# Kernel optimization log

Measured on AMD Instinct MI355X. Metric: run time of the kernel, lower is better.

## Reference

```python
import jax, jax.numpy as jnp
import numpy as np

B, C, S, E, H = 16, 24, 128, 256, 8
P = E // H  # head projection dim (consistent interpretation of the buggy source)
EPS = 1e-6


def _ln(x, g, b):
    mu = jnp.mean(x, axis=-1, keepdims=True)
    var = jnp.mean((x - mu) ** 2, axis=-1, keepdims=True)
    return (x - mu) * jax.lax.rsqrt(var + EPS) * g + b


def setup_inputs() -> dict:
    key = jax.random.key(0)
    ks = jax.random.split(key, 16)
    s = 0.02
    return {
        'x': jax.random.normal(ks[0], (B, C, S, E), jnp.float32),
        # spatial attention params
        'Wq_s': s * jax.random.normal(ks[1], (H, C, P, E), jnp.float32),
        'Wk_s': s * jax.random.normal(ks[2], (H, E, P), jnp.float32),
        'Wv_s': s * jax.random.normal(ks[3], (H, E, P), jnp.float32),
        'Wo_s': s * jax.random.normal(ks[4], (C, E, E), jnp.float32),
        # temporal attention params
        'Wq_t': s * jax.random.normal(ks[5], (H, C, E, P), jnp.float32),
        'Wk_t': s * jax.random.normal(ks[6], (H, C, E, P), jnp.float32),
        'Wv_t': s * jax.random.normal(ks[7], (H, C, E, P), jnp.float32),
        'Wo_t': s * jax.random.normal(ks[8], (C, E, E), jnp.float32),
        # shared layernorm
        'ln_g': jnp.ones((E,), jnp.float32),
        'ln_b': jnp.zeros((E,), jnp.float32),
        # per-joint pointwise FF (Linear->ReLU->Linear)
        'ff_w1': s * jax.random.normal(ks[9], (C, E, E), jnp.float32),
        'ff_b1': jnp.zeros((C, E), jnp.float32),
        'ff_w2': s * jax.random.normal(ks[10], (C, E, E), jnp.float32),
        'ff_b2': jnp.zeros((C, E), jnp.float32),
    }


def _spatial_attention(x, Wq, Wk, Wv, Wo):
    # x: [B,C,S,E]; per-head per-joint query proj, shared key/value proj
    q = jnp.einsum('bcse,hcpe->bshcp', x, Wq)          # [B,S,H,C,P]
    k = jnp.einsum('bcse,hep->bshcp', x, Wk)
    v = jnp.einsum('bcse,hep->bshcp', x, Wv)
    scores = jnp.einsum('bshcp,bshdp->bshcd', q, k) / jnp.sqrt(jnp.float32(P))
    a = jax.nn.softmax(scores, axis=-1)                # attn over joints d
    o = jnp.einsum('bshcd,bshdp->bshcp', a, v)
    o = o.transpose(0, 3, 1, 2, 4).reshape(x.shape[0], C, x.shape[2], H * P)  # [B,C,S,E]
    return jnp.einsum('bcse,cef->bcsf', o, Wo)


def _temporal_attention(x, Wq, Wk, Wv, Wo):
    q = jnp.einsum('bcse,hcep->bhcsp', x, Wq)          # [B,H,C,S,P]
    k = jnp.einsum('bcse,hcep->bhcsp', x, Wk)
    v = jnp.einsum('bcse,hcep->bhcsp', x, Wv)
    scores = jnp.einsum('bhcsp,bhctp->bhcst', q, k) / jnp.sqrt(jnp.float32(P))
    a = jax.nn.softmax(scores, axis=-1)                # attn over time t
    o = jnp.einsum('bhcst,bhctp->bhcsp', a, v)
    o = o.transpose(0, 2, 3, 1, 4).reshape(x.shape[0], C, x.shape[2], H * P)  # [B,C,S,E]
    return jnp.einsum('bcse,cef->bcsf', o, Wo)


def reference(x, Wq_s, Wk_s, Wv_s, Wo_s, Wq_t, Wk_t, Wv_t, Wo_t, ln_g, ln_b, ff_w1, ff_b1, ff_w2, ff_b2):
    spat = _spatial_attention(x, Wq_s, Wk_s, Wv_s, Wo_s)
    temp = _temporal_attention(x, Wq_t, Wk_t, Wv_t, Wo_t)
    attn_out = _ln(x + spat, ln_g, ln_b) + _ln(x + temp, ln_g, ln_b)
    # per-joint pointwise FF, vectorized over joints
    h = jax.nn.relu(jnp.einsum('bcse,cef->bcsf', attn_out, ff_w1) + ff_b1[None, :, None, :])
    ff = jnp.einsum('bcse,cef->bcsf', h, ff_w2) + ff_b2[None, :, None, :]
    return _ln(attn_out + ff, ln_g, ln_b)
```

## Files before the change

### kernel.cpp

```cpp
#include <hip/hip_runtime.h>
#include <hip/hip_bf16.h>

constexpr int Bn = 16, Cn = 24, Sn = 128, En = 256, Hn = 8, Pn = 32;
constexpr int NROWS = Bn * Cn * Sn;
constexpr size_t NBUF = (size_t)Bn * Cn * Sn * En;
constexpr size_t WSLOT = (size_t)Cn * 256 * 256;

typedef __bf16 bf16_t;
typedef bf16_t bf16x8 __attribute__((ext_vector_type(8)));
typedef bf16_t bf16x4 __attribute__((ext_vector_type(4)));
typedef float f32x4 __attribute__((ext_vector_type(4)));

__device__ __forceinline__ void gl2lds16(const bf16_t* g, bf16_t* l) {
    typedef const __attribute__((address_space(1))) unsigned int* gp_t;
    typedef __attribute__((address_space(3))) unsigned int* lp_t;
    __builtin_amdgcn_global_load_lds((gp_t)(unsigned long long)g,
                                     (lp_t)(unsigned int)(unsigned long long)l,
                                     16, 0, 0);
}

__global__ __launch_bounds__(256) void conv_x_k(const float* __restrict__ x,
                                                bf16_t* __restrict__ xb) {
    const size_t i = ((size_t)blockIdx.x * 256 + threadIdx.x) * 4;
    const float4 v = *(const float4*)(x + i);
    bf16x4 o = {(bf16_t)v.x, (bf16_t)v.y, (bf16_t)v.z, (bf16_t)v.w};
    *(bf16x4*)(xb + i) = o;
}

__global__ __launch_bounds__(256) void conv_w_copy_k(const float* __restrict__ W,
                                                     bf16_t* __restrict__ out) {
    const int row = blockIdx.x * 4 + (threadIdx.x >> 6);
    const int lane = threadIdx.x & 63;
    const int n = row & 255, c = row >> 8;
    const float* src = W + (size_t)c * (Pn * En) + (size_t)(n >> 5) * (Cn * Pn * En) +
                       (size_t)(n & 31) * En + lane * 4;
    const float4 v = *(const float4*)src;
    bf16x4 o = {(bf16_t)v.x, (bf16_t)v.y, (bf16_t)v.z, (bf16_t)v.w};
    *(bf16x4*)(out + (size_t)row * 256 + lane * 4) = o;
}

struct TDesc { const float* W; int Sc, Snh, Se; };

__global__ __launch_bounds__(256) void conv_w_tr_k(
    TDesc d0, TDesc d1, TDesc d2, TDesc d3, TDesc d4, TDesc d5, TDesc d6,
    bf16_t* __restrict__ out)
{
    TDesc d;
    switch (blockIdx.z) {
        case 0: d = d0; break; case 1: d = d1; break; case 2: d = d2; break;
        case 3: d = d3; break; case 4: d = d4; break; case 5: d = d5; break;
        default: d = d6; break;
    }
    const int g = blockIdx.x & 7, et = blockIdx.x >> 3;
    const int c = blockIdx.y;

    __shared__ float tile[32][65];

    const int t = threadIdx.x;
    const float* base = d.W + (size_t)c * d.Sc + (size_t)g * d.Snh;

#pragma unroll
    for (int pass = 0; pass < 2; ++pass) {
        const int e_local = pass * 32 + (t >> 3);
        const int j4 = (t & 7) * 4;
        const float4 v = *(const float4*)(base + (size_t)(et * 64 + e_local) * d.Se + j4);
        tile[j4 + 0][e_local] = v.x;
        tile[j4 + 1][e_local] = v.y;
        tile[j4 + 2][e_local] = v.z;
        tile[j4 + 3][e_local] = v.w;
    }
    __syncthreads();

    const int j = t >> 3, e8 = (t & 7) * 8;
    bf16x8 o;
#pragma unroll
    for (int k = 0; k < 8; ++k) o[k] = (bf16_t)tile[j][e8 + k];
    *(bf16x8*)(out + (size_t)blockIdx.z * WSLOT +
               ((size_t)c * 256 + g * 32 + j) * 256 + et * 64 + e8) = o;
}

__global__ __launch_bounds__(256) void conv_w_k(const float* __restrict__ W,
                                                bf16_t* __restrict__ Wb,
                                                int Sc, int Snh, int Snp, int Se) {
    const int n = blockIdx.x & 255, c = blockIdx.x >> 8;
    const int e = threadIdx.x;
    Wb[(size_t)blockIdx.x * 256 + e] =
        (bf16_t)W[(size_t)c * Sc + (size_t)(n >> 5) * Snh + (n & 31) * Snp + (size_t)e * Se];
}

struct GDesc { const bf16_t* W; bf16_t* O; int Aoff, Wc, Ob, Oc, Os, Onh, Onp, trans; };

template <int NP, int EPI>
__global__ __launch_bounds__(256) void gemm_mfma(
    const bf16_t* __restrict__ A, int Ab, int Ac, int As,
    GDesc g0, GDesc g1, GDesc g2, const float* __restrict__ bias)
{
    const int b = blockIdx.x, c = blockIdx.z;
    const int proj = (NP == 1) ? 0 : ((int)blockIdx.y >> 1);
    const int nt = (NP == 1) ? (int)blockIdx.y : ((int)blockIdx.y & 1);
    GDesc g = (proj == 0) ? g0 : (proj == 1) ? g1 : g2;

    __shared__ bf16_t smem[3][2][128 * 32];
    bf16_t* Cs = &smem[0][0][0];

    const int tid = threadIdx.x, wv = tid >> 6, ln = tid & 63;
    const int wm = (wv >> 1) * 64, wn = (wv & 1) * 64;
    const int lr = ln & 15, hi = ln >> 4;

    const bf16_t* Abase = A + g.Aoff + (size_t)b * Ab + (size_t)c * Ac;
    const bf16_t* Bbase = g.W + (size_t)c * g.Wc + (size_t)(nt * 128) * 256;

    auto stage = [&](int buf, int kt) {
        const int k0 = kt * 32;
#pragma unroll
        for (int it = 0; it < 2; ++it) {
            const int cb = it * 256 + wv * 64;
            const int mc = cb + ln;
            const int row = mc >> 2;
            const int kc = (((mc & 3) ^ ((row >> 1) & 3)) * 8);
            gl2lds16(Abase + (size_t)row * As + k0 + kc, &smem[buf][0][cb * 8]);
            gl2lds16(Bbase + (size_t)row * 256 + k0 + kc, &smem[buf][1][cb * 8]);
        }
    };

    f32x4 acc[4][4] = {};

    stage(0, 0);
    stage(1, 1);

#pragma unroll
    for (int kt = 0; kt < 8; ++kt) {
        if (kt < 6) stage((kt + 2) % 3, kt + 2);
        if (kt < 6)       asm volatile("s_waitcnt vmcnt(8)" ::: "memory");
        else if (kt == 6) asm volatile("s_waitcnt vmcnt(4)" ::: "memory");
        else              asm volatile("s_waitcnt vmcnt(0)" ::: "memory");
        __builtin_amdgcn_s_barrier();
        __builtin_amdgcn_sched_barrier(0);

        const int cur = kt % 3;
        bf16x8 af[4], bfr[4];
#pragma unroll
        for (int i = 0; i < 4; ++i) {
            const int r = wm + i * 16 + lr;
            af[i] = *(const bf16x8*)&smem[cur][0][r * 32 + ((hi ^ ((r >> 1) & 3)) * 8)];
        }
#pragma unroll
        for (int j = 0; j < 4; ++j) {
            const int r = wn + j * 16 + lr;
            bfr[j] = *(const bf16x8*)&smem[cur][1][r * 32 + ((hi ^ ((r >> 1) & 3)) * 8)];
        }
        __builtin_amdgcn_s_setprio(1);
#pragma unroll
        for (int i = 0; i < 4; ++i)
#pragma unroll
            for (int j = 0; j < 4; ++j)
                acc[i][j] = __builtin_amdgcn_mfma_f32_16x16x32_bf16(af[i], bfr[j], acc[i][j], 0, 0, 0);
        __builtin_amdgcn_s_setprio(0);

        __builtin_amdgcn_sched_barrier(0);
        __builtin_amdgcn_s_barrier();
    }

#pragma unroll
    for (int pass = 0; pass < 2; ++pass) {
        if (!g.trans) {
            if (wm == pass * 64) {
#pragma unroll
                for (int i = 0; i < 4; ++i)
#pragma unroll
                    for (int j = 0; j < 4; ++j) {
                        const int n = nt * 128 + wn + j * 16 + lr;
                        float bv = 0.f;
                        if (EPI) bv = bias[c * 256 + n];
#pragma unroll
                        for (int r = 0; r < 4; ++r) {
                            float v = acc[i][j][r];
                            if (EPI) { v += bv; if (EPI == 1) v = fmaxf(v, 0.f); }
                            Cs[(i * 16 + hi * 4 + r) * 136 + wn + j * 16 + lr] = (bf16_t)v;
                        }
                    }
            }
            __syncthreads();
#pragma unroll
            for (int it = 0; it < 2; ++it) {
                const int lrow = it * 32 + (tid >> 3);
                const int n0 = (tid & 7) * 16;
                bf16x8 v0 = *(const bf16x8*)&Cs[lrow * 136 + n0];
                bf16x8 v1 = *(const bf16x8*)&Cs[lrow * 136 + n0 + 8];
                const int m = pass * 64 + lrow;
                const int n = nt * 128 + n0;
                bf16_t* dst = g.O + (size_t)b * g.Ob + (size_t)c * g.Oc +
                              (size_t)m * g.Os + (size_t)(n >> 5) * g.Onh + (n & 31);
                *(bf16x8*)dst = v0;
                *(bf16x8*)(dst + 8) = v1;
            }
            __syncthreads();
        } else {
            if (wn == pass * 64) {
#pragma unroll
                for (int i = 0; i < 4; ++i)
#pragma unroll
                    for (int j = 0; j < 4; ++j) {
                        bf16x4 pk = {(bf16_t)acc[i][j][0], (bf16_t)acc[i][j][1],
                                     (bf16_t)acc[i][j][2], (bf16_t)acc[i][j][3]};
                        *(bf16x4*)&Cs[(j * 16 + lr) * 136 + wm + i * 16 + hi * 4] = pk;
                    }
            }
            __syncthreads();
#pragma unroll
            for (int it = 0; it < 2; ++it) {
                const int lrow = it * 32 + (tid >> 3);
                const int m0 = (tid & 7) * 16;
                bf16x8 v0 = *(const bf16x8*)&Cs[lrow * 136 + m0];
                bf16x8 v1 = *(const bf16x8*)&Cs[lrow * 136 + m0 + 8];
                const int n = nt * 128 + pass * 64 + lrow;
                bf16_t* dst = g.O + (size_t)b * g.Ob + (size_t)c * g.Oc +
                              (size_t)(n >> 5) * g.Onh + (size_t)(n & 31) * g.Onp + m0;
                *(bf16x8*)dst = v0;
                *(bf16x8*)(dst + 8) = v1;
            }
            __syncthreads();
        }
    }
}

__global__ __launch_bounds__(256) void attn_spatial_mfma(
    const bf16_t* __restrict__ Q, const bf16_t* __restrict__ K,
    const bf16_t* __restrict__ V, bf16_t* __restrict__ O)
{
    __shared__ bf16_t Ps[4][32 * 40];
    __shared__ bf16_t Vt[4][32 * 40];

    const int tid = threadIdx.x, wv = tid >> 6, ln = tid & 63;
    const int lr = ln & 15, hi = ln >> 4, lk = hi * 8;

    const int bsh = blockIdx.x * 4 + wv;
    const int h = bsh & 7, s = (bsh >> 3) & 127, b = bsh >> 10;
    const size_t qb = (size_t)bsh * (Cn * Pn);

    {
        const int p = ln >> 1, c0 = 24 + (ln & 1) * 4;
        bf16x4 z = {};
        *(bf16x4*)&Vt[wv][p * 40 + c0] = z;
    }
#pragma unroll
    for (int it = 0; it < 2; ++it) {
        const int ch = it * 64 + ln;
        if (ch < 96) {
            const int cc = ch >> 2, p0 = (ch & 3) * 8;
            bf16x8 v = *(const bf16x8*)(V + qb + cc * 32 + p0);
#pragma unroll
            for (int j = 0; j < 8; ++j)
                Vt[wv][(p0 + j) * 40 + cc] = v[j];
        }
    }

    bf16x8 aq0 = *(const bf16x8*)(Q + qb + lr * 32 + lk);
    bf16x8 aq1 = *(const bf16x8*)(Q + qb + (16 + lr) * 32 + lk);
    bf16x8 bk0 = *(const bf16x8*)(K + qb + lr * 32 + lk);
    bf16x8 bk1 = *(const bf16x8*)(K + qb + (16 + lr) * 32 + lk);
    const f32x4 zz = {0.f, 0.f, 0.f, 0.f};
    f32x4 sc[2][2];
    sc[0][0] = __builtin_amdgcn_mfma_f32_16x16x32_bf16(aq0, bk0, zz, 0, 0, 0);
    sc[0][1] = __builtin_amdgcn_mfma_f32_16x16x32_bf16(aq0, bk1, zz, 0, 0, 0);
    sc[1][0] = __builtin_amdgcn_mfma_f32_16x16x32_bf16(aq1, bk0, zz, 0, 0, 0);
    sc[1][1] = __builtin_amdgcn_mfma_f32_16x16x32_bf16(aq1, bk1, zz, 0, 0, 0);

    const float scale = 0.17677669529663687f;
#pragma unroll
    for (int i = 0; i < 2; ++i) {
        float s0[4], s1[4], mx[4];
#pragma unroll
        for (int r = 0; r < 4; ++r) {
            s0[r] = sc[i][0][r] * scale;
            s1[r] = (lr >= 8) ? -3.0e38f : sc[i][1][r] * scale;
            mx[r] = fmaxf(s0[r], s1[r]);
        }
#pragma unroll
        for (int d = 1; d < 16; d <<= 1)
#pragma unroll
            for (int r = 0; r < 4; ++r) mx[r] = fmaxf(mx[r], __shfl_xor(mx[r], d));
        float e0[4], e1[4], sm[4];
#pragma unroll
        for (int r = 0; r < 4; ++r) {
            e0[r] = __expf(s0[r] - mx[r]);
            e1[r] = __expf(s1[r] - mx[r]);
            sm[r] = e0[r] + e1[r];
        }
#pragma unroll
        for (int d = 1; d < 16; d <<= 1)
#pragma unroll
            for (int r = 0; r < 4; ++r) sm[r] += __shfl_xor(sm[r], d);
#pragma unroll
        for (int r = 0; r < 4; ++r) {
            const float inv = 1.f / sm[r];
            const int row = i * 16 + hi * 4 + r;
            Ps[wv][row * 40 + lr]      = (bf16_t)(e0[r] * inv);
            Ps[wv][row * 40 + 16 + lr] = (bf16_t)(e1[r] * inv);
        }
    }

    bf16x8 ap0 = *(const bf16x8*)&Ps[wv][lr * 40 + lk];
    bf16x8 ap1 = *(const bf16x8*)&Ps[wv][(16 + lr) * 40 + lk];
    bf16x8 bv0 = *(const bf16x8*)&Vt[wv][lr * 40 + lk];
    bf16x8 bv1 = *(const bf16x8*)&Vt[wv][(16 + lr) * 40 + lk];
    f32x4 o[2][2];
    o[0][0] = __builtin_amdgcn_mfma_f32_16x16x32_bf16(ap0, bv0, zz, 0, 0, 0);
    o[0][1] = __builtin_amdgcn_mfma_f32_16x16x32_bf16(ap0, bv1, zz, 0, 0, 0);
    o[1][0] = __builtin_amdgcn_mfma_f32_16x16x32_bf16(ap1, bv0, zz, 0, 0, 0);
    o[1][1] = __builtin_amdgcn_mfma_f32_16x16x32_bf16(ap1, bv1, zz, 0, 0, 0);

#pragma unroll
    for (int i = 0; i < 2; ++i)
#pragma unroll
        for (int r = 0; r < 4; ++r) {
            const int c = i * 16 + hi * 4 + r;
            if (c < 24) {
                const size_t ob = ((size_t)(b * Cn + c) * Sn + s) * En + h * Pn;
#pragma unroll
                for (int j = 0; j < 2; ++j)
                    O[ob + j * 16 + lr] = (bf16_t)o[i][j][r];
            }
        }
}

__global__ __launch_bounds__(256) void attn_temporal_mfma(
    const bf16_t* __restrict__ Q, const bf16_t* __restrict__ K,
    const bf16_t* __restrict__ Vt, bf16_t* __restrict__ O)
{
    const int c = blockIdx.x, h = blockIdx.y, b = blockIdx.z;
    const size_t base = ((size_t)(b * Hn + h) * Cn + c) * (Sn * Pn);

    __shared__ bf16_t Qs[128 * 32];
    __shared__ bf16_t Ks[128 * 32];
    __shared__ bf16_t Vs[32 * 136];
    __shared__ bf16_t Ps[128 * 136];

    const int tid = threadIdx.x, wv = tid >> 6, ln = tid & 63;
    const int lr = ln & 15, lk = (ln >> 4) * 8;

#pragma unroll
    for (int it = 0; it < 2; ++it) {
        const int cb = it * 256 + wv * 64;
        const int mc = cb + ln;
        const int row = mc >> 2, kc = (mc & 3) * 8;
        gl2lds16(Q + base + row * 32 + kc, &Qs[cb * 8]);
        gl2lds16(K + base + row * 32 + kc, &Ks[cb * 8]);
    }
#pragma unroll
    for (int it = 0; it < 2; ++it) {
        const int mc = it * 256 + tid;
        const int p = mc >> 4, scn = (mc & 15) * 8;
        bf16x8 v = *(const bf16x8*)(Vt + base + p * 128 + scn);
        *(bf16x8*)&Vs[p * 136 + scn] = v;
    }
    __syncthreads();

    const int r0 = wv * 32;
    bf16x8 aq0 = *(const bf16x8*)&Qs[(r0 + lr) * 32 + lk];
    bf16x8 aq1 = *(const bf16x8*)&Qs[(r0 + 16 + lr) * 32 + lk];
    f32x4 sc_[2][8];
    const f32x4 zz = {0.f, 0.f, 0.f, 0.f};
#pragma unroll
    for (int j = 0; j < 8; ++j) {
        bf16x8 bk = *(const bf16x8*)&Ks[(j * 16 + lr) * 32 + lk];
        sc_[0][j] = __builtin_amdgcn_mfma_f32_16x16x32_bf16(aq0, bk, zz, 0, 0, 0);
        sc_[1][j] = __builtin_amdgcn_mfma_f32_16x16x32_bf16(aq1, bk, zz, 0, 0, 0);
    }

    const float scale = 0.17677669529663687f;
#pragma unroll
    for (int i = 0; i < 2; ++i) {
        float mx[4], sm[4];
#pragma unroll
        for (int r = 0; r < 4; ++r) {
            float m = sc_[i][0][r];
#pragma unroll
            for (int j = 1; j < 8; ++j) m = fmaxf(m, sc_[i][j][r]);
            mx[r] = m;
        }
#pragma unroll
        for (int d = 1; d < 16; d <<= 1)
#pragma unroll
            for (int r = 0; r < 4; ++r) mx[r] = fmaxf(mx[r], __shfl_xor(mx[r], d));
#pragma unroll
        for (int r = 0; r < 4; ++r) sm[r] = 0.f;
#pragma unroll
        for (int j = 0; j < 8; ++j)
#pragma unroll
            for (int r = 0; r < 4; ++r) {
                const float e = __expf((sc_[i][j][r] - mx[r]) * scale);
                sc_[i][j][r] = e; sm[r] += e;
            }
#pragma unroll
        for (int d = 1; d < 16; d <<= 1)
#pragma unroll
            for (int r = 0; r < 4; ++r) sm[r] += __shfl_xor(sm[r], d);
        float inv[4];
#pragma unroll
        for (int r = 0; r < 4; ++r) inv[r] = 1.f / sm[r];
        const int rb = r0 + i * 16 + (ln >> 4) * 4;
#pragma unroll
        for (int j = 0; j < 8; ++j)
#pragma unroll
            for (int r = 0; r < 4; ++r)
                Ps[(rb + r) * 136 + j * 16 + lr] = (bf16_t)(sc_[i][j][r] * inv[r]);
    }
    __syncthreads();

    f32x4 o[2][2] = {};
#pragma unroll
    for (int kk = 0; kk < 4; ++kk) {
        bf16x8 ap0 = *(const bf16x8*)&Ps[(r0 + lr) * 136 + kk * 32 + lk];
        bf16x8 ap1 = *(const bf16x8*)&Ps[(r0 + 16 + lr) * 136 + kk * 32 + lk];
        bf16x8 bv0 = *(const bf16x8*)&Vs[lr * 136 + kk * 32 + lk];
        bf16x8 bv1 = *(const bf16x8*)&Vs[(16 + lr) * 136 + kk * 32 + lk];
        o[0][0] = __builtin_amdgcn_mfma_f32_16x16x32_bf16(ap0, bv0, o[0][0], 0, 0, 0);
        o[0][1] = __builtin_amdgcn_mfma_f32_16x16x32_bf16(ap0, bv1, o[0][1], 0, 0, 0);
        o[1][0] = __builtin_amdgcn_mfma_f32_16x16x32_bf16(ap1, bv0, o[1][0], 0, 0, 0);
        o[1][1] = __builtin_amdgcn_mfma_f32_16x16x32_bf16(ap1, bv1, o[1][1], 0, 0, 0);
    }

#pragma unroll
    for (int i = 0; i < 2; ++i) {
        const int sb = r0 + i * 16 + (ln >> 4) * 4;
#pragma unroll
        for (int j = 0; j < 2; ++j) {
            const int p = h * 32 + j * 16 + lr;
#pragma unroll
            for (int r = 0; r < 4; ++r)
                O[((size_t)(b * Cn + c) * Sn + (sb + r)) * En + p] = (bf16_t)o[i][j][r];
        }
    }
}

__global__ __launch_bounds__(256) void ln_combine_k(
    const bf16_t* __restrict__ xb, const bf16_t* __restrict__ spat,
    const bf16_t* __restrict__ temp, const float* __restrict__ g,
    const float* __restrict__ beta, bf16_t* __restrict__ AO)
{
    const int row = blockIdx.x * 4 + (threadIdx.x >> 6);
    const int lane = threadIdx.x & 63;
    const size_t off = (size_t)row * En;

    float v1[4], v2[4];
    float s1 = 0, s2 = 0, q1 = 0, q2 = 0;
#pragma unroll
    for (int i = 0; i < 4; i++) {
        const int e = lane + i * 64;
        const float xv = (float)xb[off + e];
        const float a = xv + (float)spat[off + e];
        const float t = xv + (float)temp[off + e];
        v1[i] = a; v2[i] = t;
        s1 += a; s2 += t; q1 += a * a; q2 += t * t;
    }
    for (int d = 32; d; d >>= 1) {
        s1 += __shfl_xor(s1, d); s2 += __shfl_xor(s2, d);
        q1 += __shfl_xor(q1, d); q2 += __shfl_xor(q2, d);
    }
    const float mu1 = s1 / En, mu2 = s2 / En;
    const float r1 = rsqrtf(q1 / En - mu1 * mu1 + 1e-6f);
    const float r2 = rsqrtf(q2 / En - mu2 * mu2 + 1e-6f);
#pragma unroll
    for (int i = 0; i < 4; i++) {
        const int e = lane + i * 64;
        const float out = (v1[i] - mu1) * r1 * g[e] + beta[e] +
                          (v2[i] - mu2) * r2 * g[e] + beta[e];
        AO[off + e] = (bf16_t)out;
    }
}

__global__ __launch_bounds__(256) void ln_final_k(
    const bf16_t* __restrict__ AO, const bf16_t* __restrict__ FF,
    const float* __restrict__ g, const float* __restrict__ beta,
    float* __restrict__ out)
{
    const int row = blockIdx.x * 4 + (threadIdx.x >> 6);
    const int lane = threadIdx.x & 63;
    const size_t off = (size_t)row * En;

    float v[4];
    float s = 0, q = 0;
#pragma unroll
    for (int i = 0; i < 4; i++) {
        const int e = lane + i * 64;
        const float a = (float)AO[off + e] + (float)FF[off + e];
        v[i] = a; s += a; q += a * a;
    }
    for (int d = 32; d; d >>= 1) { s += __shfl_xor(s, d); q += __shfl_xor(q, d); }
    const float mu = s / En;
    const float r = rsqrtf(q / En - mu * mu + 1e-6f);
#pragma unroll
    for (int i = 0; i < 4; i++) {
        const int e = lane + i * 64;
        out[off + e] = (v[i] - mu) * r * g[e] + beta[e];
    }
}

extern "C" void kernel_launch(void* const* d_in, const int* in_sizes, int n_in,
                              void* d_out, int out_size, void* d_ws, size_t ws_size,
                              hipStream_t stream)
{
    const float* x     = (const float*)d_in[0];
    const float* Wq_s  = (const float*)d_in[1];
    const float* Wk_s  = (const float*)d_in[2];
    const float* Wv_s  = (const float*)d_in[3];
    const float* Wo_s  = (const float*)d_in[4];
    const float* Wq_t  = (const float*)d_in[5];
    const float* Wk_t  = (const float*)d_in[6];
    const float* Wv_t  = (const float*)d_in[7];
    const float* Wo_t  = (const float*)d_in[8];
    const float* ln_g  = (const float*)d_in[9];
    const float* ln_b  = (const float*)d_in[10];
    const float* ff_w1 = (const float*)d_in[11];
    const float* ff_b1 = (const float*)d_in[12];
    const float* ff_w2 = (const float*)d_in[13];
    const float* ff_b2 = (const float*)d_in[14];
    float* out = (float*)d_out;

    bf16_t* wsb = (bf16_t*)d_ws;
    bf16_t* b0 = wsb;
    bf16_t* b1 = wsb + NBUF;
    bf16_t* b2 = wsb + 2 * NBUF;
    bf16_t* b3 = wsb + 3 * NBUF;
    bf16_t* b4 = wsb + 4 * NBUF;

    bf16_t* xb = (bf16_t*)d_out;
    bf16_t* wb = xb + NBUF;
    bf16_t* w_qs = wb + 0 * WSLOT;
    bf16_t* wtr  = wb + 1 * WSLOT;
    bf16_t* w_os = wtr + 0 * WSLOT;
    bf16_t* w_qt = wtr + 1 * WSLOT;
    bf16_t* w_kt = wtr + 2 * WSLOT;
    bf16_t* w_vt = wtr + 3 * WSLOT;
    bf16_t* w_ot = wtr + 4 * WSLOT;
    bf16_t* w_f1 = wtr + 5 * WSLOT;
    bf16_t* w_f2 = wtr + 6 * WSLOT;
    bf16_t* w_ks = b4 + NBUF - 2 * 65536;
    bf16_t* w_vs = b4 + NBUF - 65536;

    const int XAb = Cn * Sn * En, XAc = Sn * En, XAs = En;
    const int QSb = Sn * Hn * Cn * Pn, QSs = Hn * Cn * Pn, QSh = Cn * Pn;
    const int QTb = Hn * Cn * Sn * Pn, QTh = Cn * Sn * Pn, QTc = Sn * Pn, QTs = Pn;
    const int WCP = 256 * 256;

    conv_x_k<<<NBUF / 1024, 256, 0, stream>>>(x, xb);
    conv_w_copy_k<<<1536, 256, 0, stream>>>(Wq_s, w_qs);
    conv_w_tr_k<<<dim3(32, 24, 7), 256, 0, stream>>>(
        TDesc{Wo_s, En * En, Pn, En},
        TDesc{Wq_t, En * Pn, Cn * En * Pn, Pn},
        TDesc{Wk_t, En * Pn, Cn * En * Pn, Pn},
        TDesc{Wv_t, En * Pn, Cn * En * Pn, Pn},
        TDesc{Wo_t, En * En, Pn, En},
        TDesc{ff_w1, En * En, Pn, En},
        TDesc{ff_w2, En * En, Pn, En},
        wtr);
    conv_w_k<<<256, 256, 0, stream>>>(Wk_s, w_ks, 0, En * Pn, 1, Pn);
    conv_w_k<<<256, 256, 0, stream>>>(Wv_s, w_vs, 0, En * Pn, 1, Pn);

    gemm_mfma<3, 0><<<dim3(16, 6, 24), 256, 0, stream>>>(
        xb, XAb, XAc, XAs,
        GDesc{w_qs, b0, 0, WCP, QSb, Pn, QSs, QSh, 1, 0},
        GDesc{w_ks, b1, 0, 0,   QSb, Pn, QSs, QSh, 1, 0},
        GDesc{w_vs, b2, 0, 0,   QSb, Pn, QSs, QSh, 1, 0},
        nullptr);
    attn_spatial_mfma<<<Bn * Sn * Hn / 4, 256, 0, stream>>>(b0, b1, b2, b3);

    gemm_mfma<3, 0><<<dim3(16, 6, 24), 256, 0, stream>>>(
        xb, XAb, XAc, XAs,
        GDesc{w_qt, b0, 0, WCP, QTb, QTc, QTs, QTh, 1, 0},
        GDesc{w_kt, b1, 0, WCP, QTb, QTc, QTs, QTh, 1, 0},
        GDesc{w_vt, b2, 0, WCP, QTb, QTc, 1, QTh, Sn, 1},
        nullptr);
    attn_temporal_mfma<<<dim3(24, 8, 16), 256, 0, stream>>>(b0, b1, b2, b4);

    gemm_mfma<2, 0><<<dim3(16, 4, 24), 256, 0, stream>>>(
        b3, XAb, XAc, XAs,
        GDesc{w_os, b0, 0,          WCP, XAb, XAc, XAs, 32, 1, 0},
        GDesc{w_ot, b1, (int)NBUF,  WCP, XAb, XAc, XAs, 32, 1, 0},
        GDesc{w_os, b0, 0,          WCP, XAb, XAc, XAs, 32, 1, 0}, nullptr);

    ln_combine_k<<<NROWS / 4, 256, 0, stream>>>(xb, b0, b1, ln_g, ln_b, b2);
    gemm_mfma<1, 1><<<dim3(16, 2, 24), 256, 0, stream>>>(
        b2, XAb, XAc, XAs,
        GDesc{w_f1, b3, 0, WCP, XAb, XAc, XAs, 32, 1, 0},
        GDesc{w_f1, b3, 0, WCP, XAb, XAc, XAs, 32, 1, 0},
        GDesc{w_f1, b3, 0, WCP, XAb, XAc, XAs, 32, 1, 0}, ff_b1);
    gemm_mfma<1, 2><<<dim3(16, 2, 24), 256, 0, stream>>>(
        b3, XAb, XAc, XAs,
        GDesc{w_f2, b4, 0, WCP, XAb, XAc, XAs, 32, 1, 0},
        GDesc{w_f2, b4, 0, WCP, XAb, XAc, XAs, 32, 1, 0},
        GDesc{w_f2, b4, 0, WCP, XAb, XAc, XAs, 32, 1, 0}, ff_b2);
    ln_final_k<<<NROWS / 4, 256, 0, stream>>>(b2, b4, ln_g, ln_b, out);
}
```

Before: 388.4 us.

## Fuse output projections with LayerNorm and fuse both FF GEMMs with final LayerNorm

Replaces the combined Wo GEMM plus the separate ln_combine kernel with one kernel. That kernel computes both spatial and temporal output projections for a 64-row by 256-column tile and applies the two LayerNorms in its epilogue. The FF1, ReLU, FF2 and final LayerNorm chain also becomes one kernel, with the hidden activation kept in LDS, so the bf16 intermediates no longer round-trip through global memory. The FF weight conversion moves later into a freed scratch buffer, and the generic GEMM loses its bias epilogue. The cost is a small grid of 768 blocks, each covering full rows, which may lower parallelism and occupancy because of the large LDS use.

```diff
diff --git a/kernel.cpp b/kernel.cpp
--- a/kernel.cpp
+++ b/kernel.cpp
@@ -2,7 +2,6 @@
 #include <hip/hip_bf16.h>
 
 constexpr int Bn = 16, Cn = 24, Sn = 128, En = 256, Hn = 8, Pn = 32;
-constexpr int NROWS = Bn * Cn * Sn;
 constexpr size_t NBUF = (size_t)Bn * Cn * Sn * En;
 constexpr size_t WSLOT = (size_t)Cn * 256 * 256;
 
@@ -42,14 +41,13 @@
 struct TDesc { const float* W; int Sc, Snh, Se; };
 
 __global__ __launch_bounds__(256) void conv_w_tr_k(
-    TDesc d0, TDesc d1, TDesc d2, TDesc d3, TDesc d4, TDesc d5, TDesc d6,
+    TDesc d0, TDesc d1, TDesc d2, TDesc d3, TDesc d4,
     bf16_t* __restrict__ out)
 {
     TDesc d;
     switch (blockIdx.z) {
         case 0: d = d0; break; case 1: d = d1; break; case 2: d = d2; break;
-        case 3: d = d3; break; case 4: d = d4; break; case 5: d = d5; break;
-        default: d = d6; break;
+        case 3: d = d3; break; default: d = d4; break;
     }
     const int g = blockIdx.x & 7, et = blockIdx.x >> 3;
     const int c = blockIdx.y;
@@ -90,10 +88,10 @@
 
 struct GDesc { const bf16_t* W; bf16_t* O; int Aoff, Wc, Ob, Oc, Os, Onh, Onp, trans; };
 
-template <int NP, int EPI>
+template <int NP>
 __global__ __launch_bounds__(256) void gemm_mfma(
     const bf16_t* __restrict__ A, int Ab, int Ac, int As,
-    GDesc g0, GDesc g1, GDesc g2, const float* __restrict__ bias)
+    GDesc g0, GDesc g1, GDesc g2)
 {
     const int b = blockIdx.x, c = blockIdx.z;
     const int proj = (NP == 1) ? 0 : ((int)blockIdx.y >> 1);
@@ -168,17 +166,11 @@
 #pragma unroll
                 for (int i = 0; i < 4; ++i)
 #pragma unroll
-                    for (int j = 0; j < 4; ++j) {
-                        const int n = nt * 128 + wn + j * 16 + lr;
-                        float bv = 0.f;
-                        if (EPI) bv = bias[c * 256 + n];
-#pragma unroll
-                        for (int r = 0; r < 4; ++r) {
-                            float v = acc[i][j][r];
-                            if (EPI) { v += bv; if (EPI == 1) v = fmaxf(v, 0.f); }
-                            Cs[(i * 16 + hi * 4 + r) * 136 + wn + j * 16 + lr] = (bf16_t)v;
-                        }
-                    }
+                    for (int j = 0; j < 4; ++j)
+#pragma unroll
+                        for (int r = 0; r < 4; ++r)
+                            Cs[(i * 16 + hi * 4 + r) * 136 + wn + j * 16 + lr] =
+                                (bf16_t)acc[i][j][r];
             }
             __syncthreads();
 #pragma unroll
@@ -224,6 +216,315 @@
     }
 }
 
+__global__ __launch_bounds__(256) void wo_ln_fused(
+    const bf16_t* __restrict__ A1, const bf16_t* __restrict__ A2,
+    const bf16_t* __restrict__ W1, const bf16_t* __restrict__ W2,
+    const bf16_t* __restrict__ xb, const float* __restrict__ g,
+    const float* __restrict__ beta, bf16_t* __restrict__ AO)
+{
+    const int bx = blockIdx.x, c = blockIdx.z;
+    const int R = ((bx >> 1) * Cn + c) * Sn + (bx & 1) * 64;
+
+    __shared__ bf16_t lds[33792];
+
+    const int tid = threadIdx.x, wv = tid >> 6, ln = tid & 63;
+    const int wn = wv * 64, lr = ln & 15, hi = ln >> 4;
+
+    const bf16_t* Ab0 = A1 + (size_t)R * 256;
+    const bf16_t* Ab1 = A2 + (size_t)R * 256;
+    const bf16_t* Wb0 = W1 + (size_t)c * 65536;
+    const bf16_t* Wb1 = W2 + (size_t)c * 65536;
+
+    auto stage = [&](int buf, int t) {
+        const bf16_t* Asrc = (t < 8) ? Ab0 : Ab1;
+        const bf16_t* Wsrc = (t < 8) ? Wb0 : Wb1;
+        const int k0 = (t & 7) * 32;
+        bf16_t* base = &lds[buf * 10240];
+        {
+            const int ch = wv * 64 + ln;
+            const int row = ch >> 2;
+            const int kc = (((ch & 3) ^ ((row >> 1) & 3)) * 8);
+            gl2lds16(Asrc + (size_t)row * 256 + k0 + kc, base + ch * 8);
+        }
+#pragma unroll
+        for (int g2 = 0; g2 < 4; ++g2) {
+            const int ch = g2 * 256 + wv * 64 + ln;
+            const int row = ch >> 2;
+            const int kc = (((ch & 3) ^ ((row >> 1) & 3)) * 8);
+            gl2lds16(Wsrc + (size_t)row * 256 + k0 + kc, base + 2048 + ch * 8);
+        }
+    };
+
+    f32x4 accS[4][4] = {}, accT[4][4] = {};
+
+    stage(0, 0);
+#pragma unroll
+    for (int t = 0; t < 16; ++t) {
+        if (t < 15) {
+            stage((t + 1) & 1, t + 1);
+            asm volatile("s_waitcnt vmcnt(5)" ::: "memory");
+        } else {
+            asm volatile("s_waitcnt vmcnt(0)" ::: "memory");
+        }
+        __builtin_amdgcn_s_barrier();
+        __builtin_amdgcn_sched_barrier(0);
+
+        const bf16_t* base = &lds[(t & 1) * 10240];
+        bf16x8 af[4], bfr[4];
+#pragma unroll
+        for (int i = 0; i < 4; ++i) {
+            const int r = i * 16 + lr;
+            af[i] = *(const bf16x8*)(base + r * 32 + ((hi ^ ((r >> 1) & 3)) * 8));
+        }
+#pragma unroll
+        for (int j = 0; j < 4; ++j) {
+            const int r = wn + j * 16 + lr;
+            bfr[j] = *(const bf16x8*)(base + 2048 + r * 32 + ((hi ^ ((r >> 1) & 3)) * 8));
+        }
+        __builtin_amdgcn_s_setprio(1);
+        if (t < 8) {
+#pragma unroll
+            for (int i = 0; i < 4; ++i)
+#pragma unroll
+                for (int j = 0; j < 4; ++j)
+                    accS[i][j] = __builtin_amdgcn_mfma_f32_16x16x32_bf16(af[i], bfr[j], accS[i][j], 0, 0, 0);
+        } else {
+#pragma unroll
+            for (int i = 0; i < 4; ++i)
+#pragma unroll
+                for (int j = 0; j < 4; ++j)
+                    accT[i][j] = __builtin_amdgcn_mfma_f32_16x16x32_bf16(af[i], bfr[j], accT[i][j], 0, 0, 0);
+        }
+        __builtin_amdgcn_s_setprio(0);
+        __builtin_amdgcn_sched_barrier(0);
+        __builtin_amdgcn_s_barrier();
+    }
+
+    bf16_t* Ss = &lds[0];
+    bf16_t* Ts = &lds[16896];
+#pragma unroll
+    for (int i = 0; i < 4; ++i)
+#pragma unroll
+        for (int j = 0; j < 4; ++j)
+#pragma unroll
+            for (int r = 0; r < 4; ++r) {
+                const int m = i * 16 + hi * 4 + r;
+                const int n = wn + j * 16 + lr;
+                Ss[m * 264 + n] = (bf16_t)accS[i][j][r];
+                Ts[m * 264 + n] = (bf16_t)accT[i][j][r];
+            }
+    __syncthreads();
+
+    const int row = tid >> 2, c0 = (tid & 3) * 64;
+    const bf16_t* xp = xb + (size_t)(R + row) * 256 + c0;
+    bf16x8 xv[8];
+    float s1 = 0, q1 = 0, s2 = 0, q2 = 0;
+#pragma unroll
+    for (int u = 0; u < 8; ++u) {
+        xv[u] = *(const bf16x8*)(xp + u * 8);
+        bf16x8 sv = *(const bf16x8*)&Ss[row * 264 + c0 + u * 8];
+        bf16x8 tv = *(const bf16x8*)&Ts[row * 264 + c0 + u * 8];
+#pragma unroll
+        for (int e = 0; e < 8; ++e) {
+            const float xf = (float)xv[u][e];
+            const float a = xf + (float)sv[e];
+            const float t2 = xf + (float)tv[e];
+            s1 += a; q1 += a * a; s2 += t2; q2 += t2 * t2;
+        }
+    }
+    s1 += __shfl_xor(s1, 1); s1 += __shfl_xor(s1, 2);
+    q1 += __shfl_xor(q1, 1); q1 += __shfl_xor(q1, 2);
+    s2 += __shfl_xor(s2, 1); s2 += __shfl_xor(s2, 2);
+    q2 += __shfl_xor(q2, 1); q2 += __shfl_xor(q2, 2);
+    const float mu1 = s1 / 256.f, mu2 = s2 / 256.f;
+    const float r1 = rsqrtf(q1 / 256.f - mu1 * mu1 + 1e-6f);
+    const float r2 = rsqrtf(q2 / 256.f - mu2 * mu2 + 1e-6f);
+#pragma unroll
+    for (int u = 0; u < 8; ++u) {
+        bf16x8 sv = *(const bf16x8*)&Ss[row * 264 + c0 + u * 8];
+        bf16x8 tv = *(const bf16x8*)&Ts[row * 264 + c0 + u * 8];
+        bf16x8 o8;
+#pragma unroll
+        for (int e = 0; e < 8; ++e) {
+            const int n = c0 + u * 8 + e;
+            const float xf = (float)xv[u][e];
+            const float a = xf + (float)sv[e];
+            const float t2 = xf + (float)tv[e];
+            o8[e] = (bf16_t)((a - mu1) * r1 * g[n] + (t2 - mu2) * r2 * g[n] + 2.f * beta[n]);
+        }
+        *(bf16x8*)(AO + (size_t)(R + row) * 256 + c0 + u * 8) = o8;
+    }
+}
+
+__global__ __launch_bounds__(256) void ff_ln_fused(
+    const bf16_t* __restrict__ AO, const bf16_t* __restrict__ W1,
+    const bf16_t* __restrict__ W2, const float* __restrict__ b1v,
+    const float* __restrict__ b2v, const float* __restrict__ g,
+    const float* __restrict__ beta, float* __restrict__ out)
+{
+    const int bx = blockIdx.x, c = blockIdx.z;
+    const int R = ((bx >> 1) * Cn + c) * Sn + (bx & 1) * 64;
+
+    __shared__ bf16_t lds[37376];
+
+    const int tid = threadIdx.x, wv = tid >> 6, ln = tid & 63;
+    const int wn = wv * 64, lr = ln & 15, hi = ln >> 4;
+
+    const bf16_t* Abase = AO + (size_t)R * 256;
+    const bf16_t* W1b = W1 + (size_t)c * 65536;
+    const bf16_t* W2b = W2 + (size_t)c * 65536;
+    bf16_t* Hs = &lds[20480];
+
+    auto stageA = [&](int buf, int kt) {
+        const int k0 = kt * 32;
+        const int ch = wv * 64 + ln;
+        const int row = ch >> 2;
+        const int kc = (((ch & 3) ^ ((row >> 1) & 3)) * 8);
+        gl2lds16(Abase + (size_t)row * 256 + k0 + kc, &lds[buf * 10240] + ch * 8);
+    };
+    auto stageB = [&](int buf, int kt, const bf16_t* Wsrc) {
+        const int k0 = kt * 32;
+#pragma unroll
+        for (int g2 = 0; g2 < 4; ++g2) {
+            const int ch = g2 * 256 + wv * 64 + ln;
+            const int row = ch >> 2;
+            const int kc = (((ch & 3) ^ ((row >> 1) & 3)) * 8);
+            gl2lds16(Wsrc + (size_t)row * 256 + k0 + kc, &lds[buf * 10240] + 2048 + ch * 8);
+        }
+    };
+
+    f32x4 acc[4][4] = {};
+
+    stageA(0, 0); stageB(0, 0, W1b);
+#pragma unroll
+    for (int t = 0; t < 8; ++t) {
+        if (t < 7) {
+            stageA((t + 1) & 1, t + 1); stageB((t + 1) & 1, t + 1, W1b);
+            asm volatile("s_waitcnt vmcnt(5)" ::: "memory");
+        } else {
+            asm volatile("s_waitcnt vmcnt(0)" ::: "memory");
+        }
+        __builtin_amdgcn_s_barrier();
+        __builtin_amdgcn_sched_barrier(0);
+        const bf16_t* base = &lds[(t & 1) * 10240];
+        bf16x8 af[4], bfr[4];
+#pragma unroll
+        for (int i = 0; i < 4; ++i) {
+            const int r = i * 16 + lr;
+            af[i] = *(const bf16x8*)(base + r * 32 + ((hi ^ ((r >> 1) & 3)) * 8));
+        }
+#pragma unroll
+        for (int j = 0; j < 4; ++j) {
+            const int r = wn + j * 16 + lr;
+            bfr[j] = *(const bf16x8*)(base + 2048 + r * 32 + ((hi ^ ((r >> 1) & 3)) * 8));
+        }
+        __builtin_amdgcn_s_setprio(1);
+#pragma unroll
+        for (int i = 0; i < 4; ++i)
+#pragma unroll
+            for (int j = 0; j < 4; ++j)
+                acc[i][j] = __builtin_amdgcn_mfma_f32_16x16x32_bf16(af[i], bfr[j], acc[i][j], 0, 0, 0);
+        __builtin_amdgcn_s_setprio(0);
+        __builtin_amdgcn_sched_barrier(0);
+        __builtin_amdgcn_s_barrier();
+    }
+
+    stageB(0, 0, W2b);
+#pragma unroll
+    for (int i = 0; i < 4; ++i)
+#pragma unroll
+        for (int j = 0; j < 4; ++j) {
+            const int n = wn + j * 16 + lr;
+            const float bv = b1v[c * 256 + n];
+#pragma unroll
+            for (int r = 0; r < 4; ++r)
+                Hs[(i * 16 + hi * 4 + r) * 264 + n] =
+                    (bf16_t)fmaxf(acc[i][j][r] + bv, 0.f);
+        }
+    __syncthreads();
+
+    f32x4 acc2[4][4] = {};
+#pragma unroll
+    for (int t = 0; t < 8; ++t) {
+        if (t < 7) {
+            stageB((t + 1) & 1, t + 1, W2b);
+            asm volatile("s_waitcnt vmcnt(4)" ::: "memory");
+        } else {
+            asm volatile("s_waitcnt vmcnt(0)" ::: "memory");
+        }
+        __builtin_amdgcn_s_barrier();
+        __builtin_amdgcn_sched_barrier(0);
+        const bf16_t* base = &lds[(t & 1) * 10240];
+        bf16x8 af[4], bfr[4];
+#pragma unroll
+        for (int i = 0; i < 4; ++i)
+            af[i] = *(const bf16x8*)&Hs[(i * 16 + lr) * 264 + t * 32 + hi * 8];
+#pragma unroll
+        for (int j = 0; j < 4; ++j) {
+            const int r = wn + j * 16 + lr;
+            bfr[j] = *(const bf16x8*)(base + 2048 + r * 32 + ((hi ^ ((r >> 1) & 3)) * 8));
+        }
+        __builtin_amdgcn_s_setprio(1);
+#pragma unroll
+        for (int i = 0; i < 4; ++i)
+#pragma unroll
+            for (int j = 0; j < 4; ++j)
+                acc2[i][j] = __builtin_amdgcn_mfma_f32_16x16x32_bf16(af[i], bfr[j], acc2[i][j], 0, 0, 0);
+        __builtin_amdgcn_s_setprio(0);
+        __builtin_amdgcn_sched_barrier(0);
+        __builtin_amdgcn_s_barrier();
+    }
+
+    bf16_t* Fs = &lds[0];
+#pragma unroll
+    for (int i = 0; i < 4; ++i)
+#pragma unroll
+        for (int j = 0; j < 4; ++j) {
+            const int n = wn + j * 16 + lr;
+            const float bv = b2v[c * 256 + n];
+#pragma unroll
+            for (int r = 0; r < 4; ++r)
+                Fs[(i * 16 + hi * 4 + r) * 264 + n] = (bf16_t)(acc2[i][j][r] + bv);
+        }
+    __syncthreads();
+
+    const int row = tid >> 2, c0 = (tid & 3) * 64;
+    const bf16_t* ap = AO + (size_t)(R + row) * 256 + c0;
+    bf16x8 av[8];
+    float s = 0, q = 0;
+#pragma unroll
+    for (int u = 0; u < 8; ++u) {
+        av[u] = *(const bf16x8*)(ap + u * 8);
+        bf16x8 fv = *(const bf16x8*)&Fs[row * 264 + c0 + u * 8];
+#pragma unroll
+        for (int e = 0; e < 8; ++e) {
+            const float a = (float)av[u][e] + (float)fv[e];
+            s += a; q += a * a;
+        }
+    }
+    s += __shfl_xor(s, 1); s += __shfl_xor(s, 2);
+    q += __shfl_xor(q, 1); q += __shfl_xor(q, 2);
+    const float mu = s / 256.f;
+    const float rin = rsqrtf(q / 256.f - mu * mu + 1e-6f);
+#pragma unroll
+    for (int u = 0; u < 8; ++u) {
+        bf16x8 fv = *(const bf16x8*)&Fs[row * 264 + c0 + u * 8];
+        float4 o0, o1;
+        float* op = &o0.x;
+#pragma unroll
+        for (int e = 0; e < 8; ++e) {
+            const int n = c0 + u * 8 + e;
+            const float a = (float)av[u][e] + (float)fv[e];
+            const float v = (a - mu) * rin * g[n] + beta[n];
+            if (e < 4) (&o0.x)[e] = v; else (&o1.x)[e - 4] = v;
+        }
+        (void)op;
+        float* dst = out + (size_t)(R + row) * 256 + c0 + u * 8;
+        *(float4*)dst = o0;
+        *(float4*)(dst + 4) = o1;
+    }
+}
+
 __global__ __launch_bounds__(256) void attn_spatial_mfma(
     const bf16_t* __restrict__ Q, const bf16_t* __restrict__ K,
     const bf16_t* __restrict__ V, bf16_t* __restrict__ O)
@@ -431,69 +732,6 @@
             for (int r = 0; r < 4; ++r)
                 O[((size_t)(b * Cn + c) * Sn + (sb + r)) * En + p] = (bf16_t)o[i][j][r];
         }
-    }
-}
-
-__global__ __launch_bounds__(256) void ln_combine_k(
-    const bf16_t* __restrict__ xb, const bf16_t* __restrict__ spat,
-    const bf16_t* __restrict__ temp, const float* __restrict__ g,
-    const float* __restrict__ beta, bf16_t* __restrict__ AO)
-{
-    const int row = blockIdx.x * 4 + (threadIdx.x >> 6);
-    const int lane = threadIdx.x & 63;
-    const size_t off = (size_t)row * En;
-
-    float v1[4], v2[4];
-    float s1 = 0, s2 = 0, q1 = 0, q2 = 0;
-#pragma unroll
-    for (int i = 0; i < 4; i++) {
-        const int e = lane + i * 64;
-        const float xv = (float)xb[off + e];
-        const float a = xv + (float)spat[off + e];
-        const float t = xv + (float)temp[off + e];
-        v1[i] = a; v2[i] = t;
-        s1 += a; s2 += t; q1 += a * a; q2 += t * t;
-    }
-    for (int d = 32; d; d >>= 1) {
-        s1 += __shfl_xor(s1, d); s2 += __shfl_xor(s2, d);
-        q1 += __shfl_xor(q1, d); q2 += __shfl_xor(q2, d);
-    }
-    const float mu1 = s1 / En, mu2 = s2 / En;
-    const float r1 = rsqrtf(q1 / En - mu1 * mu1 + 1e-6f);
-    const float r2 = rsqrtf(q2 / En - mu2 * mu2 + 1e-6f);
-#pragma unroll
-    for (int i = 0; i < 4; i++) {
-        const int e = lane + i * 64;
-        const float out = (v1[i] - mu1) * r1 * g[e] + beta[e] +
-                          (v2[i] - mu2) * r2 * g[e] + beta[e];
-        AO[off + e] = (bf16_t)out;
-    }
-}
-
-__global__ __launch_bounds__(256) void ln_final_k(
-    const bf16_t* __restrict__ AO, const bf16_t* __restrict__ FF,
-    const float* __restrict__ g, const float* __restrict__ beta,
-    float* __restrict__ out)
-{
-    const int row = blockIdx.x * 4 + (threadIdx.x >> 6);
-    const int lane = threadIdx.x & 63;
-    const size_t off = (size_t)row * En;
-
-    float v[4];
-    float s = 0, q = 0;
-#pragma unroll
-    for (int i = 0; i < 4; i++) {
-        const int e = lane + i * 64;
-        const float a = (float)AO[off + e] + (float)FF[off + e];
-        v[i] = a; s += a; q += a * a;
-    }
-    for (int d = 32; d; d >>= 1) { s += __shfl_xor(s, d); q += __shfl_xor(q, d); }
-    const float mu = s / En;
-    const float r = rsqrtf(q / En - mu * mu + 1e-6f);
-#pragma unroll
-    for (int i = 0; i < 4; i++) {
-        const int e = lane + i * 64;
-        out[off + e] = (v[i] - mu) * r * g[e] + beta[e];
     }
 }
 
@@ -534,10 +772,10 @@
     bf16_t* w_kt = wtr + 2 * WSLOT;
     bf16_t* w_vt = wtr + 3 * WSLOT;
     bf16_t* w_ot = wtr + 4 * WSLOT;
-    bf16_t* w_f1 = wtr + 5 * WSLOT;
-    bf16_t* w_f2 = wtr + 6 * WSLOT;
     bf16_t* w_ks = b4 + NBUF - 2 * 65536;
     bf16_t* w_vs = b4 + NBUF - 65536;
+    bf16_t* w_f1 = b0;
+    bf16_t* w_f2 = b0 + WSLOT;
 
     const int XAb = Cn * Sn * En, XAc = Sn * En, XAs = En;
     const int QSb = Sn * Hn * Cn * Pn, QSs = Hn * Cn * Pn, QSh = Cn * Pn;
@@ -546,50 +784,41 @@
 
     conv_x_k<<<NBUF / 1024, 256, 0, stream>>>(x, xb);
     conv_w_copy_k<<<1536, 256, 0, stream>>>(Wq_s, w_qs);
-    conv_w_tr_k<<<dim3(32, 24, 7), 256, 0, stream>>>(
+    conv_w_tr_k<<<dim3(32, 24, 5), 256, 0, stream>>>(
         TDesc{Wo_s, En * En, Pn, En},
         TDesc{Wq_t, En * Pn, Cn * En * Pn, Pn},
         TDesc{Wk_t, En * Pn, Cn * En * Pn, Pn},
         TDesc{Wv_t, En * Pn, Cn * En * Pn, Pn},
         TDesc{Wo_t, En * En, Pn, En},
-        TDesc{ff_w1, En * En, Pn, En},
-        TDesc{ff_w2, En * En, Pn, En},
         wtr);
     conv_w_k<<<256, 256, 0, stream>>>(Wk_s, w_ks, 0, En * Pn, 1, Pn);
     conv_w_k<<<256, 256, 0, stream>>>(Wv_s, w_vs, 0, En * Pn, 1, Pn);
 
-    gemm_mfma<3, 0><<<dim3(16, 6, 24), 256, 0, stream>>>(
+    gemm_mfma<3><<<dim3(16, 6, 24), 256, 0, stream>>>(
         xb, XAb, XAc, XAs,
         GDesc{w_qs, b0, 0, WCP, QSb, Pn, QSs, QSh, 1, 0},
         GDesc{w_ks, b1, 0, 0,   QSb, Pn, QSs, QSh, 1, 0},
-        GDesc{w_vs, b2, 0, 0,   QSb, Pn, QSs, QSh, 1, 0},
-        nullptr);
+        GDesc{w_vs, b2, 0, 0,   QSb, Pn, QSs, QSh, 1, 0});
     attn_spatial_mfma<<<Bn * Sn * Hn / 4, 256, 0, stream>>>(b0, b1, b2, b3);
 
-    gemm_mfma<3, 0><<<dim3(16, 6, 24), 256, 0, stream>>>(
+    gemm_mfma<3><<<dim3(16, 6, 24), 256, 0, stream>>>(
         xb, XAb, XAc, XAs,
         GDesc{w_qt, b0, 0, WCP, QTb, QTc, QTs, QTh, 1, 0},
         GDesc{w_kt, b1, 0, WCP, QTb, QTc, QTs, QTh, 1, 0},
-        GDesc{w_vt, b2, 0, WCP, QTb, QTc, 1, QTh, Sn, 1},
-        nullptr);
+        GDesc{w_vt, b2, 0, WCP, QTb, QTc, 1, QTh, Sn, 1});
     attn_temporal_mfma<<<dim3(24, 8, 16), 256, 0, stream>>>(b0, b1, b2, b4);
 
-    gemm_mfma<2, 0><<<dim3(16, 4, 24), 256, 0, stream>>>(
-        b3, XAb, XAc, XAs,
-        GDesc{w_os, b0, 0,          WCP, XAb, XAc, XAs, 32, 1, 0},
-        GDesc{w_ot, b1, (int)NBUF,  WCP, XAb, XAc, XAs, 32, 1, 0},
-        GDesc{w_os, b0, 0,          WCP, XAb, XAc, XAs, 32, 1, 0}, nullptr);
-
-    ln_combine_k<<<NROWS / 4, 256, 0, stream>>>(xb, b0, b1, ln_g, ln_b, b2);
-    gemm_mfma<1, 1><<<dim3(16, 2, 24), 256, 0, stream>>>(
-        b2, XAb, XAc, XAs,
-        GDesc{w_f1, b3, 0, WCP, XAb, XAc, XAs, 32, 1, 0},
-        GDesc{w_f1, b3, 0, WCP, XAb, XAc, XAs, 32, 1, 0},
-        GDesc{w_f1, b3, 0, WCP, XAb, XAc, XAs, 32, 1, 0}, ff_b1);
-    gemm_mfma<1, 2><<<dim3(16, 2, 24), 256, 0, stream>>>(
-        b3, XAb, XAc, XAs,
-        GDesc{w_f2, b4, 0, WCP, XAb, XAc, XAs, 32, 1, 0},
-        GDesc{w_f2, b4, 0, WCP, XAb, XAc, XAs, 32, 1, 0},
-        GDesc{w_f2, b4, 0, WCP, XAb, XAc, XAs, 32, 1, 0}, ff_b2);
-    ln_final_k<<<NROWS / 4, 256, 0, stream>>>(b2, b4, ln_g, ln_b, out);
-}
+    conv_w_tr_k<<<dim3(32, 24, 2), 256, 0, stream>>>(
+        TDesc{ff_w1, En * En, Pn, En},
+        TDesc{ff_w2, En * En, Pn, En},
+        TDesc{ff_w1, En * En, Pn, En},
+        TDesc{ff_w1, En * En, Pn, En},
+        TDesc{ff_w1, En * En, Pn, En},
+        w_f1);
+
+    wo_ln_fused<<<dim3(32, 1, 24), 256, 0, stream>>>(
+        b3, b4, w_os, w_ot, xb, ln_g, ln_b, b2);
+
+    ff_ln_fused<<<dim3(32, 1, 24), 256, 0, stream>>>(
+        b2, w_f1, w_f2, ff_b1, ff_b2, ln_g, ln_b, out);
+}
```

Measured after the change: 387.3 us. About the same (-0.3%).
